# Kernel optimization log

Hardware: AMD Instinct MI355X
Metric: run time of the kernel (lower is better)

Reference implementation:

```python
import jax, jax.numpy as jnp
import numpy as np

B, T, C, H = 4, 4096, 1024, 64

def setup_inputs() -> dict:
    key = jax.random.key(0)
    k1, k2, k3, k4 = jax.random.split(key, 4)
    x = jax.random.normal(k1, (B, T, C), dtype=jnp.float32)
    # Linear(n_embed, head_size, bias=False), stored as [in, out] for x @ W
    s = 1.0 / np.sqrt(C)
    Wq = jax.random.uniform(k2, (C, H), dtype=jnp.float32, minval=-s, maxval=s)
    Wk = jax.random.uniform(k3, (C, H), dtype=jnp.float32, minval=-s, maxval=s)
    Wv = jax.random.uniform(k4, (C, H), dtype=jnp.float32, minval=-s, maxval=s)
    return {"x": x, "Wq": Wq, "Wk": Wk, "Wv": Wv}

def reference(x, Wq, Wk, Wv):
    Bn, Tn, Cn = x.shape
    q = x @ Wq  # [B,T,H]
    k = x @ Wk  # [B,T,H]
    v = x @ Wv  # [B,T,H]
    # NOTE: original scales by C**-0.5 (embedding dim), not head_size**-0.5
    wei = jnp.einsum('bqh,bkh->bqk', q, k) * (Cn ** -0.5)  # [B,T,T]
    causal = jnp.tril(jnp.ones((Tn, Tn), dtype=bool))
    wei = jnp.where(causal, wei, -jnp.inf)
    wei = jax.nn.softmax(wei, axis=-1)
    out = jnp.einsum('bqk,bkh->bqh', wei, v)  # [B,T,H]
    return out
```

## Files before the change

kernel.cpp:

```cpp
#include <hip/hip_runtime.h>
#include <hip/hip_bf16.h>


#define B_DIM 4
#define T_DIM 4096
#define C_DIM 1024
#define H_DIM 64
#define SCALE2 0.0450842066f
#define KP 72

typedef __attribute__((ext_vector_type(8))) short bf8;
typedef __attribute__((ext_vector_type(4))) float f32x4;
typedef __attribute__((ext_vector_type(16))) float f32x16;

__device__ __forceinline__ float fast_exp2(float f) {
    return __builtin_amdgcn_exp2f(f);
}
__device__ __forceinline__ ushort f2bf(float f) {
    union { float f; uint u; } x; x.f = f;
    const uint u = x.u;
    return (ushort)((u + 0x7FFFu + ((u >> 16) & 1u)) >> 16);
}
__device__ __forceinline__ uint cvt_pk_bf16(float lo, float hi) {
    uint r;
    asm("v_cvt_pk_bf16_f32 %0, %1, %2" : "=v"(r) : "v"(lo), "v"(hi));
    return r;
}
__device__ __forceinline__ void permswapf(float& a, float& b) {
    asm volatile("v_permlane32_swap_b32 %0, %1" : "+v"(a), "+v"(b));
}
__device__ __forceinline__ void permswapu(uint& a, uint& b) {
    asm volatile("v_permlane32_swap_b32 %0, %1" : "+v"(a), "+v"(b));
}
__device__ __forceinline__ bf8 frag_from(uint w0, uint w1, uint w2, uint w3) {
    union { uint u[4]; bf8 f; } x;
    x.u[0] = w0; x.u[1] = w1; x.u[2] = w2; x.u[3] = w3;
    return x.f;
}

__global__ __launch_bounds__(256) void wt_kernel(
    const float* __restrict__ Wq, const float* __restrict__ Wk,
    const float* __restrict__ Wv, ushort* __restrict__ wtg)
{
    const int id  = blockIdx.x * 256 + threadIdx.x;
    const int col = id >> 7;
    const int k8  = (id & 127) * 8;
    const int m   = col >> 6, lc = col & 63;
    const float* W = (m == 0) ? Wq : (m == 1) ? Wk : Wv;
    ushort o[8];
    #pragma unroll
    for (int i = 0; i < 8; ++i)
        o[i] = f2bf(W[(size_t)(k8 + i) * H_DIM + lc]);
    *(bf8*)&wtg[(size_t)col * C_DIM + k8] = *(bf8*)o;
}

__global__ __launch_bounds__(256) void qkv_mfma_kernel(
    const float* __restrict__ x, const ushort* __restrict__ wtg,
    ushort* __restrict__ qo, ushort* __restrict__ ko, ushort* __restrict__ vo)
{
    __shared__ ushort xs[32][KP];
    __shared__ ushort wts[192][KP];
    const int t    = threadIdx.x;
    const int lane = t & 63, wave = t >> 6;
    const int g    = lane >> 4, lid = lane & 15;
    const size_t r0 = (size_t)blockIdx.x * 32;

    f32x4 acc[2][3] = {};

    const int xrow = t >> 3, xcol = (t & 7) * 8;
    float4 xr[2];
    bf8 wreg[6];

    xr[0] = *(const float4*)&x[(r0 + xrow) * C_DIM + xcol];
    xr[1] = *(const float4*)&x[(r0 + xrow) * C_DIM + xcol + 4];
    #pragma unroll
    for (int it = 0; it < 6; ++it) {
        const int n = t + it * 256;
        wreg[it] = *(const bf8*)&wtg[(size_t)(n >> 3) * C_DIM + (n & 7) * 8];
    }

    for (int kc = 0; kc < C_DIM / 64; ++kc) {
        __syncthreads();
        {
            uint p[4];
            p[0] = cvt_pk_bf16(xr[0].x, xr[0].y); p[1] = cvt_pk_bf16(xr[0].z, xr[0].w);
            p[2] = cvt_pk_bf16(xr[1].x, xr[1].y); p[3] = cvt_pk_bf16(xr[1].z, xr[1].w);
            *(bf8*)&xs[xrow][xcol] = *(bf8*)p;
            #pragma unroll
            for (int it = 0; it < 6; ++it) {
                const int n = t + it * 256;
                *(bf8*)&wts[n >> 3][(n & 7) * 8] = wreg[it];
            }
        }
        __syncthreads();
        if (kc + 1 < C_DIM / 64) {
            const int kb = (kc + 1) * 64;
            xr[0] = *(const float4*)&x[(r0 + xrow) * C_DIM + kb + xcol];
            xr[1] = *(const float4*)&x[(r0 + xrow) * C_DIM + kb + xcol + 4];
            #pragma unroll
            for (int it = 0; it < 6; ++it) {
                const int n = t + it * 256;
                wreg[it] = *(const bf8*)&wtg[(size_t)(n >> 3) * C_DIM + kb + (n & 7) * 8];
            }
        }
        #pragma unroll
        for (int ks = 0; ks < 2; ++ks) {
            const bf8 a0 = *(const bf8*)&xs[lid][ks * 32 + g * 8];
            const bf8 a1 = *(const bf8*)&xs[16 + lid][ks * 32 + g * 8];
            #pragma unroll
            for (int j = 0; j < 3; ++j) {
                const int ct = wave * 3 + j;
                const bf8 bb = *(const bf8*)&wts[ct * 16 + lid][ks * 32 + g * 8];
                acc[0][j] = __builtin_amdgcn_mfma_f32_16x16x32_bf16(a0, bb, acc[0][j], 0, 0, 0);
                acc[1][j] = __builtin_amdgcn_mfma_f32_16x16x32_bf16(a1, bb, acc[1][j], 0, 0, 0);
            }
        }
    }

    #pragma unroll
    for (int rt = 0; rt < 2; ++rt)
        #pragma unroll
        for (int j = 0; j < 3; ++j) {
            const int ct = wave * 3 + j;
            const int m  = ct >> 2, lc = (ct & 3) * 16 + lid;
            ushort* dst = (m == 0) ? qo : (m == 1) ? ko : vo;
            const float sc = (m == 0) ? SCALE2 : 1.f;
            #pragma unroll
            for (int r = 0; r < 4; ++r) {
                const size_t row = r0 + rt * 16 + 4 * g + r;
                dst[row * H_DIM + lc] = f2bf(acc[rt][j][r] * sc);
            }
        }
}

__global__ __launch_bounds__(256) void flash_mfma_kernel(
    const ushort* __restrict__ q, const ushort* __restrict__ k,
    const ushort* __restrict__ v, float* __restrict__ pO,
    float* __restrict__ pl, float* __restrict__ out,
    int S, int nslots, int direct)
{
    const int qt  = 31 - blockIdx.y;
    const int c   = blockIdx.x;
    const int ntk = 2 * qt + 2;
    const int kt_begin = c * S;
    const int kt_end   = min((c + 1) * S, ntk);
    if (kt_begin >= kt_end) return;

    __shared__ ushort ks[64][KP];
    __shared__ ushort vt[64][KP];
    __shared__ float  lsh[4][32];

    const int t    = threadIdx.x;
    const int lane = t & 63, wave = t >> 6;
    const int l31  = lane & 31, hi = lane >> 5;
    const int b    = blockIdx.z;
    const int qrow0 = qt * 128 + wave * 32;
    const int ktw_max = (qrow0 + 31) >> 6;
    const size_t base = (size_t)b * T_DIM * H_DIM;

    bf8 qf[4];
    {
        const size_t qoff = base + (size_t)(qrow0 + l31) * H_DIM + hi * 8;
        #pragma unroll
        for (int kk = 0; kk < 4; ++kk)
            qf[kk] = *(const bf8*)&q[qoff + kk * 16];
    }

    f32x16 oa0 = {}, oa1 = {};
    float l_run = 0.f;

    const int krow = t >> 2, kc16 = (t & 3) * 16;
    const int vj = (t & 31) * 2, vc = (t >> 5) * 8;
    bf8 kr0, kr1, vr0, vr1;
    {
        const int kg = kt_begin * 64;
        kr0 = *(const bf8*)&k[base + (size_t)(kg + krow) * H_DIM + kc16];
        kr1 = *(const bf8*)&k[base + (size_t)(kg + krow) * H_DIM + kc16 + 8];
        vr0 = *(const bf8*)&v[base + (size_t)(kg + vj) * H_DIM + vc];
        vr1 = *(const bf8*)&v[base + (size_t)(kg + vj + 1) * H_DIM + vc];
    }

    #define BUILD_PA(dst, sv, bofs) do {                                   \
        uint a0_ = cvt_pk_bf16(sv[(bofs)+0], sv[(bofs)+1]);                \
        uint b0_ = cvt_pk_bf16(sv[(bofs)+4], sv[(bofs)+5]);                \
        uint a1_ = cvt_pk_bf16(sv[(bofs)+2], sv[(bofs)+3]);                \
        uint b1_ = cvt_pk_bf16(sv[(bofs)+6], sv[(bofs)+7]);                \
        permswapu(a0_, b0_); permswapu(a1_, b1_);                          \
        dst = frag_from(a0_, a1_, b0_, b1_);                               \
    } while (0)

    for (int kt64 = kt_begin; kt64 < kt_end; ++kt64) {
        __syncthreads();
        *(bf8*)&ks[krow][kc16]     = kr0;
        *(bf8*)&ks[krow][kc16 + 8] = kr1;
        #pragma unroll
        for (int i = 0; i < 8; ++i) {
            const uint pk = (uint)(ushort)vr0[i] | ((uint)(ushort)vr1[i] << 16);
            *(uint*)&vt[vc + i][vj] = pk;
        }
        __syncthreads();
        if (kt64 + 1 < kt_end) {
            const int kg = (kt64 + 1) * 64;
            kr0 = *(const bf8*)&k[base + (size_t)(kg + krow) * H_DIM + kc16];
            kr1 = *(const bf8*)&k[base + (size_t)(kg + krow) * H_DIM + kc16 + 8];
            vr0 = *(const bf8*)&v[base + (size_t)(kg + vj) * H_DIM + vc];
            vr1 = *(const bf8*)&v[base + (size_t)(kg + vj + 1) * H_DIM + vc];
        }
        if (kt64 > ktw_max) continue;

        f32x16 st0 = {}, st1 = {};
        #pragma unroll
        for (int kk = 0; kk < 4; ++kk) {
            const bf8 kfa = *(const bf8*)&ks[l31][kk * 16 + hi * 8];
            st0 = __builtin_amdgcn_mfma_f32_32x32x16_bf16(kfa, qf[kk], st0, 0, 0, 0);
        }
        #pragma unroll
        for (int kk = 0; kk < 4; ++kk) {
            const bf8 kfb = *(const bf8*)&ks[32 + l31][kk * 16 + hi * 8];
            st1 = __builtin_amdgcn_mfma_f32_32x32x16_bf16(kfb, qf[kk], st1, 0, 0, 0);
        }

        if (kt64 * 64 + 63 > qrow0) {
            const int qg  = qrow0 + l31;
            const int kb0 = kt64 * 64 + 4 * hi;
            #pragma unroll
            for (int r = 0; r < 16; ++r) {
                const int key0 = kb0 + (r & 3) + 8 * (r >> 2);
                if (key0 > qg)      st0[r] = -1e30f;
                if (key0 + 32 > qg) st1[r] = -1e30f;
            }
        }

        #pragma unroll
        for (int r = 0; r < 16; ++r) st0[r] = fast_exp2(st0[r]);
        #pragma unroll
        for (int r = 0; r < 16; ++r) st1[r] = fast_exp2(st1[r]);

        float sr[8];
        #pragma unroll
        for (int r = 0; r < 8; ++r)
            sr[r] = (st0[r] + st0[r + 8]) + (st1[r] + st1[r + 8]);
        #pragma unroll
        for (int off = 4; off > 0; off >>= 1)
            #pragma unroll
            for (int r = 0; r < 4; ++r)
                if (r < off) sr[r] += sr[r + off];
        float ls = sr[0];
        { float la = ls, lb = ls; permswapf(la, lb); ls = la + lb; }
        l_run += ls;

        bf8 pa[4];
        BUILD_PA(pa[0], st0, 0);
        BUILD_PA(pa[1], st0, 8);
        BUILD_PA(pa[2], st1, 0);
        BUILD_PA(pa[3], st1, 8);

        #pragma unroll
        for (int kk = 0; kk < 4; ++kk) {
            const bf8 vb0 = *(const bf8*)&vt[l31][kk * 16 + hi * 8];
            const bf8 vb1 = *(const bf8*)&vt[32 + l31][kk * 16 + hi * 8];
            oa0 = __builtin_amdgcn_mfma_f32_32x32x16_bf16(pa[kk], vb0, oa0, 0, 0, 0);
            oa1 = __builtin_amdgcn_mfma_f32_32x32x16_bf16(pa[kk], vb1, oa1, 0, 0, 0);
        }
    }
    #undef BUILD_PA

    if (direct) {
        if (lane < 32) lsh[wave][l31] = l_run;
        #pragma unroll
        for (int j = 0; j < 4; ++j) {
            const float4 lv = *(const float4*)&lsh[wave][8 * j + 4 * hi];
            const float iv[4] = {1.f / lv.x, 1.f / lv.y, 1.f / lv.z, 1.f / lv.w};
            #pragma unroll
            for (int rr = 0; rr < 4; ++rr) {
                const size_t rowoff = base + (size_t)(qrow0 + 8 * j + 4 * hi + rr) * H_DIM;
                out[rowoff + l31]      = oa0[4 * j + rr] * iv[rr];
                out[rowoff + 32 + l31] = oa1[4 * j + rr] * iv[rr];
            }
        }
    } else {
        const size_t u = ((size_t)b * 32 + qt) * nslots + c;
        float* po = pO + u * 8192;
        #pragma unroll
        for (int j = 0; j < 4; ++j)
            #pragma unroll
            for (int rr = 0; rr < 4; ++rr) {
                const int row = wave * 32 + 8 * j + 4 * hi + rr;
                po[(size_t)row * 64 + l31]      = oa0[4 * j + rr];
                po[(size_t)row * 64 + 32 + l31] = oa1[4 * j + rr];
            }
        if (lane < 32)
            pl[u * 128 + wave * 32 + l31] = l_run;
    }
}

__global__ __launch_bounds__(256) void combine_kernel(
    const float* __restrict__ pO, const float* __restrict__ pl,
    float* __restrict__ out, int S, int nslots)
{
    const int qt = blockIdx.x, b = blockIdx.y;
    const int ntk = 2 * qt + 2;
    const int nch = min(nslots, (ntk + S - 1) / S);
    const int t = threadIdx.x;
    const int row = t >> 1, seg = (t & 1) * 32;
    const size_t u0 = ((size_t)b * 32 + qt) * nslots;

    float L = 0.f;
    float4 o[8] = {};
    for (int cc = 0; cc < nch; ++cc) {
        L += pl[(u0 + cc) * 128 + row];
        #pragma unroll
        for (int j = 0; j < 8; ++j) {
            const float4 p = *(const float4*)&pO[(u0 + cc) * 8192 +
                                                 (size_t)row * 64 + seg + j * 4];
            o[j].x += p.x; o[j].y += p.y;
            o[j].z += p.z; o[j].w += p.w;
        }
    }
    const float inv = 1.f / L;
    const size_t ob = (size_t)b * T_DIM * H_DIM + (size_t)(qt * 128 + row) * H_DIM + seg;
    #pragma unroll
    for (int j = 0; j < 8; ++j) {
        float4 r;
        r.x = o[j].x * inv; r.y = o[j].y * inv;
        r.z = o[j].z * inv; r.w = o[j].w * inv;
        *(float4*)&out[ob + j * 4] = r;
    }
}

extern "C" void kernel_launch(void* const* d_in, const int* in_sizes, int n_in,
                              void* d_out, int out_size, void* d_ws, size_t ws_size,
                              hipStream_t stream)
{
    const float* x  = (const float*)d_in[0];
    const float* Wq = (const float*)d_in[1];
    const float* Wk = (const float*)d_in[2];
    const float* Wv = (const float*)d_in[3];
    float* out = (float*)d_out;

    const size_t MB = 1u << 20;
    char* ws = (char*)d_ws;
    ushort* qb  = (ushort*)(ws);
    ushort* kb  = (ushort*)(ws + 2 * MB);
    ushort* vb  = (ushort*)(ws + 4 * MB);
    ushort* wtg = (ushort*)(ws + 6 * MB);
    float*  pO  = (float*)(ws + 7 * MB);

    int nslots, S;
    if      (ws_size >= 80 * MB) { nslots = 16; S = 4; }
    else if (ws_size >= 41 * MB) { nslots = 8;  S = 8; }
    else if (ws_size >= 24 * MB) { nslots = 4;  S = 16; }
    else                         { nslots = 1;  S = 64; }
    const int direct = (nslots == 1);
    float* pl = pO + (size_t)nslots * 1048576;

    hipLaunchKernelGGL(wt_kernel, dim3(96), dim3(256), 0, stream, Wq, Wk, Wv, wtg);
    hipLaunchKernelGGL(qkv_mfma_kernel, dim3((B_DIM * T_DIM) / 32), dim3(256),
                       0, stream, x, wtg, qb, kb, vb);
    hipLaunchKernelGGL(flash_mfma_kernel, dim3(nslots, T_DIM / 128, B_DIM), dim3(256),
                       0, stream, qb, kb, vb, pO, pl, out, S, nslots, direct);
    if (!direct)
        hipLaunchKernelGGL(combine_kernel, dim3(T_DIM / 128, B_DIM), dim3(256),
                           0, stream, pO, pl, out, S, nslots);
}
```

Measured before the change: 72.04 us.

## Enlarge flash attention query tile to 256 rows with 8-wave blocks

Flash kernel blocks now cover 256 query rows with 512 threads (8 waves) instead of 128 rows with 4 waves. Each K/V tile staged in shared memory is reused by twice as many waves, and each thread loads half as much K/V. The partial-output layout and the combine kernel are reindexed to match. The trade-off is fewer blocks in the grid, coarser causal load balance, and higher register pressure under the 512-thread launch bound.

```diff
diff --git a/kernel.cpp b/kernel.cpp
--- a/kernel.cpp
+++ b/kernel.cpp
@@ -10,6 +10,7 @@
 #define KP 72
 
 typedef __attribute__((ext_vector_type(8))) short bf8;
+typedef __attribute__((ext_vector_type(4))) short bf4;
 typedef __attribute__((ext_vector_type(4))) float f32x4;
 typedef __attribute__((ext_vector_type(16))) float f32x16;
 
@@ -133,28 +134,28 @@
         }
 }
 
-__global__ __launch_bounds__(256) void flash_mfma_kernel(
+__global__ __launch_bounds__(512) void flash_mfma_kernel(
     const ushort* __restrict__ q, const ushort* __restrict__ k,
     const ushort* __restrict__ v, float* __restrict__ pO,
     float* __restrict__ pl, float* __restrict__ out,
     int S, int nslots, int direct)
 {
-    const int qt  = 31 - blockIdx.y;
+    const int qt  = 15 - blockIdx.y;
     const int c   = blockIdx.x;
-    const int ntk = 2 * qt + 2;
+    const int ntk = 4 * qt + 4;
     const int kt_begin = c * S;
     const int kt_end   = min((c + 1) * S, ntk);
     if (kt_begin >= kt_end) return;
 
     __shared__ ushort ks[64][KP];
     __shared__ ushort vt[64][KP];
-    __shared__ float  lsh[4][32];
+    __shared__ float  lsh[8][32];
 
     const int t    = threadIdx.x;
     const int lane = t & 63, wave = t >> 6;
     const int l31  = lane & 31, hi = lane >> 5;
     const int b    = blockIdx.z;
-    const int qrow0 = qt * 128 + wave * 32;
+    const int qrow0 = qt * 256 + wave * 32;
     const int ktw_max = (qrow0 + 31) >> 6;
     const size_t base = (size_t)b * T_DIM * H_DIM;
 
@@ -169,15 +170,15 @@
     f32x16 oa0 = {}, oa1 = {};
     float l_run = 0.f;
 
-    const int krow = t >> 2, kc16 = (t & 3) * 16;
-    const int vj = (t & 31) * 2, vc = (t >> 5) * 8;
-    bf8 kr0, kr1, vr0, vr1;
+    const int krow = t >> 3, kc8 = (t & 7) * 8;
+    const int vj = (t & 31) * 2, vc = (t >> 5) * 4;
+    bf8 krg;
+    bf4 vr0, vr1;
     {
         const int kg = kt_begin * 64;
-        kr0 = *(const bf8*)&k[base + (size_t)(kg + krow) * H_DIM + kc16];
-        kr1 = *(const bf8*)&k[base + (size_t)(kg + krow) * H_DIM + kc16 + 8];
-        vr0 = *(const bf8*)&v[base + (size_t)(kg + vj) * H_DIM + vc];
-        vr1 = *(const bf8*)&v[base + (size_t)(kg + vj + 1) * H_DIM + vc];
+        krg = *(const bf8*)&k[base + (size_t)(kg + krow) * H_DIM + kc8];
+        vr0 = *(const bf4*)&v[base + (size_t)(kg + vj) * H_DIM + vc];
+        vr1 = *(const bf4*)&v[base + (size_t)(kg + vj + 1) * H_DIM + vc];
     }
 
     #define BUILD_PA(dst, sv, bofs) do {                                   \
@@ -191,20 +192,18 @@
 
     for (int kt64 = kt_begin; kt64 < kt_end; ++kt64) {
         __syncthreads();
-        *(bf8*)&ks[krow][kc16]     = kr0;
-        *(bf8*)&ks[krow][kc16 + 8] = kr1;
-        #pragma unroll
-        for (int i = 0; i < 8; ++i) {
+        *(bf8*)&ks[krow][kc8] = krg;
+        #pragma unroll
+        for (int i = 0; i < 4; ++i) {
             const uint pk = (uint)(ushort)vr0[i] | ((uint)(ushort)vr1[i] << 16);
             *(uint*)&vt[vc + i][vj] = pk;
         }
         __syncthreads();
         if (kt64 + 1 < kt_end) {
             const int kg = (kt64 + 1) * 64;
-            kr0 = *(const bf8*)&k[base + (size_t)(kg + krow) * H_DIM + kc16];
-            kr1 = *(const bf8*)&k[base + (size_t)(kg + krow) * H_DIM + kc16 + 8];
-            vr0 = *(const bf8*)&v[base + (size_t)(kg + vj) * H_DIM + vc];
-            vr1 = *(const bf8*)&v[base + (size_t)(kg + vj + 1) * H_DIM + vc];
+            krg = *(const bf8*)&k[base + (size_t)(kg + krow) * H_DIM + kc8];
+            vr0 = *(const bf4*)&v[base + (size_t)(kg + vj) * H_DIM + vc];
+            vr1 = *(const bf4*)&v[base + (size_t)(kg + vj + 1) * H_DIM + vc];
         }
         if (kt64 > ktw_max) continue;
 
@@ -279,8 +278,8 @@
             }
         }
     } else {
-        const size_t u = ((size_t)b * 32 + qt) * nslots + c;
-        float* po = pO + u * 8192;
+        const size_t u = ((size_t)b * 16 + qt) * nslots + c;
+        float* po = pO + u * 16384;
         #pragma unroll
         for (int j = 0; j < 4; ++j)
             #pragma unroll
@@ -290,7 +289,7 @@
                 po[(size_t)row * 64 + 32 + l31] = oa1[4 * j + rr];
             }
         if (lane < 32)
-            pl[u * 128 + wave * 32 + l31] = l_run;
+            pl[u * 256 + wave * 32 + l31] = l_run;
     }
 }
 
@@ -298,27 +297,28 @@
     const float* __restrict__ pO, const float* __restrict__ pl,
     float* __restrict__ out, int S, int nslots)
 {
-    const int qt = blockIdx.x, b = blockIdx.y;
-    const int ntk = 2 * qt + 2;
+    const int qt2 = blockIdx.x, b = blockIdx.y;
+    const int qt = qt2 >> 1, half = qt2 & 1;
+    const int ntk = 4 * qt + 4;
     const int nch = min(nslots, (ntk + S - 1) / S);
     const int t = threadIdx.x;
-    const int row = t >> 1, seg = (t & 1) * 32;
-    const size_t u0 = ((size_t)b * 32 + qt) * nslots;
+    const int row = half * 128 + (t >> 1), seg = (t & 1) * 32;
+    const size_t u0 = ((size_t)b * 16 + qt) * nslots;
 
     float L = 0.f;
     float4 o[8] = {};
     for (int cc = 0; cc < nch; ++cc) {
-        L += pl[(u0 + cc) * 128 + row];
+        L += pl[(u0 + cc) * 256 + row];
         #pragma unroll
         for (int j = 0; j < 8; ++j) {
-            const float4 p = *(const float4*)&pO[(u0 + cc) * 8192 +
+            const float4 p = *(const float4*)&pO[(u0 + cc) * 16384 +
                                                  (size_t)row * 64 + seg + j * 4];
             o[j].x += p.x; o[j].y += p.y;
             o[j].z += p.z; o[j].w += p.w;
         }
     }
     const float inv = 1.f / L;
-    const size_t ob = (size_t)b * T_DIM * H_DIM + (size_t)(qt * 128 + row) * H_DIM + seg;
+    const size_t ob = (size_t)b * T_DIM * H_DIM + (size_t)(qt * 256 + row) * H_DIM + seg;
     #pragma unroll
     for (int j = 0; j < 8; ++j) {
         float4 r;
@@ -352,14 +352,14 @@
     else if (ws_size >= 24 * MB) { nslots = 4;  S = 16; }
     else                         { nslots = 1;  S = 64; }
     const int direct = (nslots == 1);
-    float* pl = pO + (size_t)nslots * 1048576;
+    float* pl = pO + (size_t)B_DIM * 16 * nslots * 16384;
 
     hipLaunchKernelGGL(wt_kernel, dim3(96), dim3(256), 0, stream, Wq, Wk, Wv, wtg);
     hipLaunchKernelGGL(qkv_mfma_kernel, dim3((B_DIM * T_DIM) / 32), dim3(256),
                        0, stream, x, wtg, qb, kb, vb);
-    hipLaunchKernelGGL(flash_mfma_kernel, dim3(nslots, T_DIM / 128, B_DIM), dim3(256),
+    hipLaunchKernelGGL(flash_mfma_kernel, dim3(nslots, T_DIM / 256, B_DIM), dim3(512),
                        0, stream, qb, kb, vb, pO, pl, out, S, nslots, direct);
     if (!direct)
-        hipLaunchKernelGGL(combine_kernel, dim3(T_DIM / 128, B_DIM), dim3(256),
+        hipLaunchKernelGGL(combine_kernel, dim3(32, B_DIM), dim3(256),
                            0, stream, pO, pl, out, S, nslots);
 }
```

New measurement: 71.05 us. Within noise of the previous version (-1.4%).
